# Kernel optimization log

Measured on AMD Instinct MI355X. Metric: run time of the kernel, lower is better.

Reference implementation:

```python
import jax, jax.numpy as jnp
import numpy as np

B, C, N, K_NN = 16, 64, 2048, 3
OUT_C = 64


def setup_inputs() -> dict:
    key = jax.random.key(0)
    k1, k2, k3 = jax.random.split(key, 3)
    x = jax.random.normal(k1, (B, C, N), dtype=jnp.float32)
    fan_in = C * K_NN
    bound = 1.0 / np.sqrt(fan_in)
    W = jax.random.uniform(k2, (OUT_C, C, K_NN), minval=-bound, maxval=bound, dtype=jnp.float32)
    b = jax.random.uniform(k3, (OUT_C,), minval=-bound, maxval=bound, dtype=jnp.float32)
    return {"x": x, "W": W, "b": b}


def reference(x, W, b):
    # x: [B, C, N]; W: [O, C, K]; b: [O]
    K = W.shape[-1]
    # Pairwise squared distances: dist[b,i,j] = |x_i|^2 + |x_j|^2 - 2 x_i.x_j.
    # The original takes sqrt, but sqrt is monotone and the distances are only
    # used for top-k index selection, so we select on squared distances (same indices).
    norm_sq = jnp.sum(x * x, axis=1)                      # [B, N]
    dot = jnp.einsum('bcn,bcm->bnm', x, x)                # [B, N, N]
    dist_sq = norm_sq[:, :, None] + norm_sq[:, None, :] - 2.0 * dot  # [B, N, N]
    # K smallest distances per row -> neighbor indices [B, N, K]
    _, idx = jax.lax.top_k(-dist_sq, K)
    # Gather neighbors: neigh[b, c, n, k] = x[b, c, idx[b, n, k]]
    neigh = jax.vmap(lambda xb, ib: xb[:, ib])(x, idx)    # [B, C, N, K]
    # Conv1d with kernel_size == stride == K over the flattened [B, C, N*K]
    # tensor is exactly a per-window contraction over the K neighbors.
    out = jnp.einsum('bcnk,ock->bon', neigh, W) + b[None, :, None]  # [B, O, N]
    return out
```

## Files before the change

kernel.cpp:

```cpp
#include <hip/hip_runtime.h>
#include <cfloat>
#include <climits>

#define B_DIM 16
#define C_DIM 64
#define N_DIM 2048
#define O_DIM 64
#define K_NN  3

typedef __attribute__((ext_vector_type(8))) short bf16x8;
typedef __attribute__((ext_vector_type(4))) float floatx4;

__device__ __forceinline__ unsigned short f32_to_bf16_rne(float f) {
  unsigned int u = __float_as_uint(f);
  return (unsigned short)((u + 0x7fffu + ((u >> 16) & 1u)) >> 16);
}
__device__ __forceinline__ float bf16_to_f32(unsigned short h) {
  return __uint_as_float(((unsigned int)h) << 16);
}

__device__ __forceinline__ unsigned med3u(unsigned a, unsigned b, unsigned c) {
  unsigned mn = min(a, b), mx = max(a, b);
  return max(mn, min(mx, c));
}

__device__ __forceinline__ void ins4p(unsigned u, int jv, unsigned* k, int* j) {
  bool c3 = u < k[3], c2 = u < k[2], c1 = u < k[1], c0 = u < k[0];
  k[3] = c2 ? k[2] : (c3 ? u  : k[3]);
  j[3] = c2 ? j[2] : (c3 ? jv : j[3]);
  k[2] = c1 ? k[1] : (c2 ? u  : k[2]);
  j[2] = c1 ? j[1] : (c2 ? jv : j[2]);
  k[1] = c0 ? k[0] : (c1 ? u  : k[1]);
  j[1] = c0 ? j[0] : (c1 ? jv : j[1]);
  k[0] = c0 ? u  : k[0];
  j[0] = c0 ? jv : j[0];
}

__global__ __launch_bounds__(256) void prep_kernel(
    const float* __restrict__ x, float* __restrict__ xT,
    unsigned short* __restrict__ xTh, unsigned short* __restrict__ xTl,
    double* __restrict__ nd, float* __restrict__ nf,
    const float* __restrict__ W, float* __restrict__ Wt) {
  int bid = blockIdx.x;
  int t = threadIdx.x;
  if (bid >= 512) {
    int t2 = (bid - 512) * 256 + t;
    int o  = t2 / (C_DIM * K_NN);
    int ck = t2 - o * (C_DIM * K_NN);
    Wt[ck * O_DIM + o] = W[t2];
    return;
  }
  __shared__ __align__(16) float xs[C_DIM][68];
  int b  = bid >> 5;
  int n0 = (bid & 31) * 64;
  const float* xb = x + (size_t)b * C_DIM * N_DIM;
  #pragma unroll
  for (int r = 0; r < 4; ++r) {
    int idx = r * 256 + t;
    int c = idx >> 4;
    int qq = idx & 15;
    *(float4*)&xs[c][qq * 4] = *(const float4*)(xb + (size_t)c * N_DIM + n0 + qq * 4);
  }
  __syncthreads();
  int n = t >> 2, cg = t & 3;
  float v[16];
  #pragma unroll
  for (int cc = 0; cc < 16; ++cc) v[cc] = xs[cg * 16 + cc][n];
  double ps = 0.0;
  #pragma unroll
  for (int cc = 0; cc < 16; ++cc) ps = fma((double)v[cc], (double)v[cc], ps);
  ps += __shfl_xor(ps, 1, 64);
  ps += __shfl_xor(ps, 2, 64);
  size_t row = (size_t)b * N_DIM + n0 + n;
  #pragma unroll
  for (int qq = 0; qq < 4; ++qq) {
    float4 wv; wv.x = v[qq*4]; wv.y = v[qq*4+1]; wv.z = v[qq*4+2]; wv.w = v[qq*4+3];
    *(float4*)&xT[row * C_DIM + cg * 16 + qq * 4] = wv;
  }
  unsigned short hh[16], ll[16];
  #pragma unroll
  for (int cc = 0; cc < 16; ++cc) {
    hh[cc] = f32_to_bf16_rne(v[cc]);
    ll[cc] = f32_to_bf16_rne(v[cc] - bf16_to_f32(hh[cc]));
  }
  #pragma unroll
  for (int e = 0; e < 2; ++e) {
    int phys = (2 * cg + e) ^ (n & 7);
    unsigned int hp[4], lp[4];
    #pragma unroll
    for (int xk = 0; xk < 4; ++xk) {
      hp[xk] = (unsigned)hh[e*8 + 2*xk] | ((unsigned)hh[e*8 + 2*xk + 1] << 16);
      lp[xk] = (unsigned)ll[e*8 + 2*xk] | ((unsigned)ll[e*8 + 2*xk + 1] << 16);
    }
    ((uint4*)xTh)[row * 8 + phys] = *(uint4*)hp;
    ((uint4*)xTl)[row * 8 + phys] = *(uint4*)lp;
  }
  if (cg == 0) {
    nd[row] = ps;
    nf[row] = (float)ps + 512.0f;
  }
}

__global__ __launch_bounds__(256, 4) void topk_kernel(
    const unsigned short* __restrict__ xTh, const unsigned short* __restrict__ xTl,
    const float* __restrict__ nf, unsigned short* __restrict__ cand, int b_base) {
  __shared__ __align__(16) unsigned short Jh[128 * 64];
  __shared__ __align__(16) unsigned short Jl[128 * 64];
  int bid   = blockIdx.x;
  int q     = bid & 3;
  int itile = (bid >> 2) & 31;
  int b     = b_base + (bid >> 7);
  int i0    = itile * 64;
  int jq0   = q * 512;
  int t = threadIdx.x;
  int w = t >> 6, lane = t & 63, quad = lane >> 4, col = lane & 15;
  int csw = col & 7;
  const unsigned short* xh = xTh + (size_t)b * N_DIM * 64;
  const unsigned short* xl = xTl + (size_t)b * N_DIM * 64;
  const float* nfb = nf + b * N_DIM;

  bf16x8 ih[2], il[2];
  #pragma unroll
  for (int ks = 0; ks < 2; ++ks) {
    size_t row = i0 + w * 16 + col;
    int phys = (ks * 4 + quad) ^ csw;
    ih[ks] = *(const bf16x8*)(xh + row * 64 + phys * 8);
    il[ks] = *(const bf16x8*)(xl + row * 64 + phys * 8);
  }

  unsigned ck[4];
  ck[0] = ck[1] = ck[2] = ck[3] = 0xFFFFFFFFu;

  int a0 = col * 64 + ((quad ^ csw) * 8);
  int a1 = col * 64 + (((4 + quad) ^ csw) * 8);

  for (int js = 0; js < 4; ++js) {
    int j0 = jq0 + js * 128;
    __syncthreads();
    {
      const unsigned short* sh = xh + (size_t)(j0 + w * 32) * 64;
      const unsigned short* sl = xl + (size_t)(j0 + w * 32) * 64;
      unsigned short* dh = &Jh[w * 32 * 64];
      unsigned short* dl = &Jl[w * 32 * 64];
      int off = lane * 8;
      #pragma unroll
      for (int k2 = 0; k2 < 4; ++k2) {
        *(uint4*)(dh + k2 * 512 + off) = *(const uint4*)(sh + k2 * 512 + off);
        *(uint4*)(dl + k2 * 512 + off) = *(const uint4*)(sl + k2 * 512 + off);
      }
    }
    __syncthreads();

    floatx4 acc[8];
    #pragma unroll
    for (int jt = 0; jt < 8; ++jt) acc[jt] = (floatx4){0.f, 0.f, 0.f, 0.f};

    #pragma unroll
    for (int ks = 0; ks < 2; ++ks) {
      int ab = ks ? a1 : a0;
      #pragma unroll
      for (int jt = 0; jt < 8; ++jt) {
        bf16x8 jh = *(const bf16x8*)&Jh[jt * 1024 + ab];
        bf16x8 jl = *(const bf16x8*)&Jl[jt * 1024 + ab];
        acc[jt] = __builtin_amdgcn_mfma_f32_16x16x32_bf16(jl, ih[ks], acc[jt], 0, 0, 0);
        acc[jt] = __builtin_amdgcn_mfma_f32_16x16x32_bf16(jh, il[ks], acc[jt], 0, 0, 0);
        acc[jt] = __builtin_amdgcn_mfma_f32_16x16x32_bf16(jh, ih[ks], acc[jt], 0, 0, 0);
      }
    }

    unsigned locb = (unsigned)(js << 5);
    int jb = j0 + quad * 4;
    #pragma unroll
    for (int jt = 0; jt < 8; ++jt) {
      float4 nv = *(const float4*)(nfb + jb + jt * 16);
      float nfa[4] = {nv.x, nv.y, nv.z, nv.w};
      #pragma unroll
      for (int r = 0; r < 4; ++r) {
        float key = fmaf(-2.0f, acc[jt][r], nfa[r]);
        unsigned u = (__float_as_uint(key) & 0xFFFFFF80u) | locb |
                     (unsigned)(jt * 4 + r);
        unsigned m0 = min(ck[0], u);
        unsigned m1 = med3u(ck[0], u, ck[1]);
        unsigned m2 = med3u(ck[1], u, ck[2]);
        unsigned m3 = med3u(ck[2], u, ck[3]);
        ck[0] = m0; ck[1] = m1; ck[2] = m2; ck[3] = m3;
      }
    }
  }

  int cj[4];
  #pragma unroll
  for (int s = 0; s < 4; ++s) {
    unsigned loc = ck[s] & 127u;
    cj[s] = jq0 + (int)((loc >> 5) << 7) + (int)(((loc >> 2) & 7u) << 4) +
            (quad << 2) + (int)(loc & 3u);
  }
  #pragma unroll
  for (int m = 16; m < 64; m <<= 1) {
    unsigned tu[4]; int tj[4];
    #pragma unroll
    for (int s = 0; s < 4; ++s) {
      tu[s] = __shfl_xor(ck[s], m, 64);
      tj[s] = __shfl_xor(cj[s], m, 64);
    }
    #pragma unroll
    for (int s = 0; s < 4; ++s) ins4p(tu[s], tj[s], ck, cj);
  }
  if (quad == 0) {
    int row = b * N_DIM + i0 + w * 16 + col;
    unsigned short* cp = cand + row * 16 + q * 4;
    cp[0] = (unsigned short)cj[0];
    cp[1] = (unsigned short)cj[1];
    cp[2] = (unsigned short)cj[2];
    cp[3] = (unsigned short)cj[3];
  }
}

__global__ __launch_bounds__(256) void refine_kernel(
    const float* __restrict__ xT, const double* __restrict__ nd,
    const unsigned short* __restrict__ cand, unsigned short* __restrict__ topk) {
  int t = threadIdx.x;
  int lane = t & 63;
  int row = blockIdx.x * 4 + (t >> 6);
  int b = row >> 11;
  int n = row & (N_DIM - 1);
  int cid = lane >> 2;
  int seg = lane & 3;
  int j = cand[row * 16 + cid];
  const float* xn = xT + (((size_t)b * N_DIM + n) * C_DIM) + seg * 16;
  const float* xj = xT + (((size_t)b * N_DIM + j) * C_DIM) + seg * 16;
  double pd = 0.0;
  #pragma unroll
  for (int qq = 0; qq < 4; ++qq) {
    float4 a  = *(const float4*)(xn + qq * 4);
    float4 bb = *(const float4*)(xj + qq * 4);
    pd = fma((double)a.x, (double)bb.x, pd);
    pd = fma((double)a.y, (double)bb.y, pd);
    pd = fma((double)a.z, (double)bb.z, pd);
    pd = fma((double)a.w, (double)bb.w, pd);
  }
  pd += __shfl_xor(pd, 1, 64);
  pd += __shfl_xor(pd, 2, 64);
  double key = fma(-2.0, pd, nd[b * N_DIM + j] + 512.0);
  unsigned long long u =
      ((unsigned long long)__double_as_longlong(key) & ~2047ull) |
      (unsigned long long)(unsigned)j;
  unsigned long long v = u;
  int jout[3];
  #pragma unroll
  for (int p = 0; p < 3; ++p) {
    unsigned long long m = v;
    #pragma unroll
    for (int msk = 4; msk < 64; msk <<= 1) {
      unsigned long long o = __shfl_xor(m, msk, 64);
      m = (o < m) ? o : m;
    }
    jout[p] = (int)(m & 2047ull);
    v = (v == m) ? ~0ull : v;
  }
  if (lane == 0) {
    unsigned short* tp = topk + row * K_NN;
    tp[0] = (unsigned short)jout[0];
    tp[1] = (unsigned short)jout[1];
    tp[2] = (unsigned short)jout[2];
  }
}

#define NT   64
#define NPAD 68
__global__ __launch_bounds__(256) void conv_kernel(
    const float* __restrict__ xT, const float* __restrict__ Wt,
    const float* __restrict__ bias, const unsigned short* __restrict__ topk,
    float* __restrict__ out) {
  __shared__ __align__(16) float nb[C_DIM * K_NN][NPAD];
  int bid = blockIdx.x;
  int b  = bid >> 5;
  int n0 = (bid & 31) * NT;
  const float* xtb = xT + (size_t)b * N_DIM * C_DIM;
  const unsigned short* tk = topk + (b * N_DIM + n0) * K_NN;
  int t = threadIdx.x;

  #pragma unroll
  for (int p = 0; p < 12; ++p) {
    int u = p * 256 + t;
    int seg = u & 15;
    int r   = u >> 4;
    int k = r >> 6, n = r & 63;
    int j = tk[n * K_NN + k];
    float4 v = *(const float4*)(xtb + (size_t)j * C_DIM + seg * 4);
    nb[(seg * 4 + 0) * 3 + k][n] = v.x;
    nb[(seg * 4 + 1) * 3 + k][n] = v.y;
    nb[(seg * 4 + 2) * 3 + k][n] = v.z;
    nb[(seg * 4 + 3) * 3 + k][n] = v.w;
  }
  __syncthreads();

  int ng = t & 15, og = t >> 4;
  float acc[4][4];
  #pragma unroll
  for (int oo = 0; oo < 4; ++oo) {
    float bv = bias[(og << 2) + oo];
    #pragma unroll
    for (int nn = 0; nn < 4; ++nn) acc[oo][nn] = bv;
  }
  const float* nbp = &nb[0][0] + (ng << 2);
  const float* wtp = Wt + (og << 2);
  #pragma unroll 4
  for (int ckk = 0; ckk < C_DIM * K_NN; ++ckk) {
    float4 nv = *(const float4*)(nbp + ckk * NPAD);
    float4 wv = *(const float4*)(wtp + ckk * O_DIM);
    float na[4] = {nv.x, nv.y, nv.z, nv.w};
    float wa[4] = {wv.x, wv.y, wv.z, wv.w};
    #pragma unroll
    for (int oo = 0; oo < 4; ++oo)
      #pragma unroll
      for (int nn = 0; nn < 4; ++nn)
        acc[oo][nn] = fmaf(wa[oo], na[nn], acc[oo][nn]);
  }
  #pragma unroll
  for (int oo = 0; oo < 4; ++oo) {
    int o = (og << 2) + oo;
    float4 v; v.x = acc[oo][0]; v.y = acc[oo][1]; v.z = acc[oo][2]; v.w = acc[oo][3];
    *(float4*)&out[(size_t)(b * O_DIM + o) * N_DIM + n0 + (ng << 2)] = v;
  }
}

extern "C" void kernel_launch(void* const* d_in, const int* in_sizes, int n_in,
                              void* d_out, int out_size, void* d_ws, size_t ws_size,
                              hipStream_t stream) {
  const float* x    = (const float*)d_in[0];
  const float* W    = (const float*)d_in[1];
  const float* bias = (const float*)d_in[2];
  float* out = (float*)d_out;
  char* ws = (char*)d_ws;
  float*          xT  = (float*)ws;
  unsigned short* xTh = (unsigned short*)(ws + 8388608);
  unsigned short* xTl = (unsigned short*)(ws + 12582912);
  double*         nd  = (double*)(ws + 16777216);
  float*          nfp = (float*)(ws + 17039360);
  unsigned short* cd  = (unsigned short*)(ws + 17170432);
  unsigned short* tk  = (unsigned short*)(ws + 18219008);
  float*          Wt  = (float*)(ws + 18415616);

  prep_kernel<<<512 + 48, 256, 0, stream>>>(x, xT, xTh, xTl, nd, nfp, W, Wt);
  topk_kernel<<<8 * 32 * 4, 256, 0, stream>>>(xTh, xTl, nfp, cd, 0);
  topk_kernel<<<8 * 32 * 4, 256, 0, stream>>>(xTh, xTl, nfp, cd, 8);
  refine_kernel<<<(B_DIM * N_DIM) / 4, 256, 0, stream>>>(xT, nd, cd, tk);
  conv_kernel<<<B_DIM * (N_DIM / NT), 256, 0, stream>>>(xT, Wt, bias, tk, out);
}
```

Before: 162.6 us.

## Fuse refine into conv kernel and merge split topk launches

The two half-batch topk launches become a single launch over all batches. The refine step, which rescores the 16 candidates per row in double precision and picks the top 3, moves into the conv kernel and keeps its indices in shared memory instead of a global topk buffer. This removes two kernel launches and the global round trip for the indices. The cost is that the conv kernel now runs refine serially, 16 rows per wave, before its gather, and only 512 blocks are available to hide that latency.

```diff
diff --git a/kernel.cpp b/kernel.cpp
--- a/kernel.cpp
+++ b/kernel.cpp
@@ -103,13 +103,13 @@
 
 __global__ __launch_bounds__(256, 4) void topk_kernel(
     const unsigned short* __restrict__ xTh, const unsigned short* __restrict__ xTl,
-    const float* __restrict__ nf, unsigned short* __restrict__ cand, int b_base) {
+    const float* __restrict__ nf, unsigned short* __restrict__ cand) {
   __shared__ __align__(16) unsigned short Jh[128 * 64];
   __shared__ __align__(16) unsigned short Jl[128 * 64];
   int bid   = blockIdx.x;
   int q     = bid & 3;
   int itile = (bid >> 2) & 31;
-  int b     = b_base + (bid >> 7);
+  int b     = bid >> 7;
   int i0    = itile * 64;
   int jq0   = q * 512;
   int t = threadIdx.x;
@@ -216,82 +216,72 @@
   }
 }
 
-__global__ __launch_bounds__(256) void refine_kernel(
-    const float* __restrict__ xT, const double* __restrict__ nd,
-    const unsigned short* __restrict__ cand, unsigned short* __restrict__ topk) {
-  int t = threadIdx.x;
-  int lane = t & 63;
-  int row = blockIdx.x * 4 + (t >> 6);
-  int b = row >> 11;
-  int n = row & (N_DIM - 1);
-  int cid = lane >> 2;
-  int seg = lane & 3;
-  int j = cand[row * 16 + cid];
-  const float* xn = xT + (((size_t)b * N_DIM + n) * C_DIM) + seg * 16;
-  const float* xj = xT + (((size_t)b * N_DIM + j) * C_DIM) + seg * 16;
-  double pd = 0.0;
-  #pragma unroll
-  for (int qq = 0; qq < 4; ++qq) {
-    float4 a  = *(const float4*)(xn + qq * 4);
-    float4 bb = *(const float4*)(xj + qq * 4);
-    pd = fma((double)a.x, (double)bb.x, pd);
-    pd = fma((double)a.y, (double)bb.y, pd);
-    pd = fma((double)a.z, (double)bb.z, pd);
-    pd = fma((double)a.w, (double)bb.w, pd);
-  }
-  pd += __shfl_xor(pd, 1, 64);
-  pd += __shfl_xor(pd, 2, 64);
-  double key = fma(-2.0, pd, nd[b * N_DIM + j] + 512.0);
-  unsigned long long u =
-      ((unsigned long long)__double_as_longlong(key) & ~2047ull) |
-      (unsigned long long)(unsigned)j;
-  unsigned long long v = u;
-  int jout[3];
-  #pragma unroll
-  for (int p = 0; p < 3; ++p) {
-    unsigned long long m = v;
-    #pragma unroll
-    for (int msk = 4; msk < 64; msk <<= 1) {
-      unsigned long long o = __shfl_xor(m, msk, 64);
-      m = (o < m) ? o : m;
-    }
-    jout[p] = (int)(m & 2047ull);
-    v = (v == m) ? ~0ull : v;
-  }
-  if (lane == 0) {
-    unsigned short* tp = topk + row * K_NN;
-    tp[0] = (unsigned short)jout[0];
-    tp[1] = (unsigned short)jout[1];
-    tp[2] = (unsigned short)jout[2];
-  }
-}
-
 #define NT   64
 #define NPAD 68
 __global__ __launch_bounds__(256) void conv_kernel(
-    const float* __restrict__ xT, const float* __restrict__ Wt,
-    const float* __restrict__ bias, const unsigned short* __restrict__ topk,
+    const float* __restrict__ xT, const double* __restrict__ nd,
+    const unsigned short* __restrict__ cand,
+    const float* __restrict__ Wt, const float* __restrict__ bias,
     float* __restrict__ out) {
   __shared__ __align__(16) float nb[C_DIM * K_NN][NPAD];
+  __shared__ unsigned short tks[NT][4];
   int bid = blockIdx.x;
   int b  = bid >> 5;
   int n0 = (bid & 31) * NT;
   const float* xtb = xT + (size_t)b * N_DIM * C_DIM;
-  const unsigned short* tk = topk + (b * N_DIM + n0) * K_NN;
   int t = threadIdx.x;
+  int w = t >> 6, lane = t & 63;
+  int cid = lane >> 2, seg = lane & 3;
+
+  for (int it = 0; it < 16; ++it) {
+    int nn = w * 16 + it;
+    int row = b * N_DIM + n0 + nn;
+    int j = cand[row * 16 + cid];
+    const float* xn = xtb + ((size_t)(n0 + nn) * C_DIM) + seg * 16;
+    const float* xj = xtb + ((size_t)j * C_DIM) + seg * 16;
+    double pd = 0.0;
+    #pragma unroll
+    for (int qq = 0; qq < 4; ++qq) {
+      float4 a  = *(const float4*)(xn + qq * 4);
+      float4 bb = *(const float4*)(xj + qq * 4);
+      pd = fma((double)a.x, (double)bb.x, pd);
+      pd = fma((double)a.y, (double)bb.y, pd);
+      pd = fma((double)a.z, (double)bb.z, pd);
+      pd = fma((double)a.w, (double)bb.w, pd);
+    }
+    pd += __shfl_xor(pd, 1, 64);
+    pd += __shfl_xor(pd, 2, 64);
+    double key = fma(-2.0, pd, nd[b * N_DIM + j] + 512.0);
+    unsigned long long u =
+        ((unsigned long long)__double_as_longlong(key) & ~2047ull) |
+        (unsigned long long)(unsigned)j;
+    unsigned long long v = u;
+    #pragma unroll
+    for (int p = 0; p < 3; ++p) {
+      unsigned long long m = v;
+      #pragma unroll
+      for (int msk = 4; msk < 64; msk <<= 1) {
+        unsigned long long o = __shfl_xor(m, msk, 64);
+        m = (o < m) ? o : m;
+      }
+      if (lane == 0) tks[nn][p] = (unsigned short)(m & 2047ull);
+      v = (v == m) ? ~0ull : v;
+    }
+  }
+  __syncthreads();
 
   #pragma unroll
   for (int p = 0; p < 12; ++p) {
     int u = p * 256 + t;
-    int seg = u & 15;
-    int r   = u >> 4;
+    int sg = u & 15;
+    int r  = u >> 4;
     int k = r >> 6, n = r & 63;
-    int j = tk[n * K_NN + k];
-    float4 v = *(const float4*)(xtb + (size_t)j * C_DIM + seg * 4);
-    nb[(seg * 4 + 0) * 3 + k][n] = v.x;
-    nb[(seg * 4 + 1) * 3 + k][n] = v.y;
-    nb[(seg * 4 + 2) * 3 + k][n] = v.z;
-    nb[(seg * 4 + 3) * 3 + k][n] = v.w;
+    int j = tks[n][k];
+    float4 v = *(const float4*)(xtb + (size_t)j * C_DIM + sg * 4);
+    nb[(sg * 4 + 0) * 3 + k][n] = v.x;
+    nb[(sg * 4 + 1) * 3 + k][n] = v.y;
+    nb[(sg * 4 + 2) * 3 + k][n] = v.z;
+    nb[(sg * 4 + 3) * 3 + k][n] = v.w;
   }
   __syncthreads();
 
@@ -301,7 +291,7 @@
   for (int oo = 0; oo < 4; ++oo) {
     float bv = bias[(og << 2) + oo];
     #pragma unroll
-    for (int nn = 0; nn < 4; ++nn) acc[oo][nn] = bv;
+    for (int nn2 = 0; nn2 < 4; ++nn2) acc[oo][nn2] = bv;
   }
   const float* nbp = &nb[0][0] + (ng << 2);
   const float* wtp = Wt + (og << 2);
@@ -314,8 +304,8 @@
     #pragma unroll
     for (int oo = 0; oo < 4; ++oo)
       #pragma unroll
-      for (int nn = 0; nn < 4; ++nn)
-        acc[oo][nn] = fmaf(wa[oo], na[nn], acc[oo][nn]);
+      for (int nn2 = 0; nn2 < 4; ++nn2)
+        acc[oo][nn2] = fmaf(wa[oo], na[nn2], acc[oo][nn2]);
   }
   #pragma unroll
   for (int oo = 0; oo < 4; ++oo) {
@@ -339,12 +329,9 @@
   double*         nd  = (double*)(ws + 16777216);
   float*          nfp = (float*)(ws + 17039360);
   unsigned short* cd  = (unsigned short*)(ws + 17170432);
-  unsigned short* tk  = (unsigned short*)(ws + 18219008);
-  float*          Wt  = (float*)(ws + 18415616);
+  float*          Wt  = (float*)(ws + 18219008);
 
   prep_kernel<<<512 + 48, 256, 0, stream>>>(x, xT, xTh, xTl, nd, nfp, W, Wt);
-  topk_kernel<<<8 * 32 * 4, 256, 0, stream>>>(xTh, xTl, nfp, cd, 0);
-  topk_kernel<<<8 * 32 * 4, 256, 0, stream>>>(xTh, xTl, nfp, cd, 8);
-  refine_kernel<<<(B_DIM * N_DIM) / 4, 256, 0, stream>>>(xT, nd, cd, tk);
-  conv_kernel<<<B_DIM * (N_DIM / NT), 256, 0, stream>>>(xT, Wt, bias, tk, out);
-}
+  topk_kernel<<<B_DIM * 32 * 4, 256, 0, stream>>>(xTh, xTl, nfp, cd);
+  conv_kernel<<<B_DIM * (N_DIM / NT), 256, 0, stream>>>(xT, nd, cd, Wt, bias, out);
+}
```

After: 162.1 us. Within noise of the previous version (-0.3%).
